# Kernel optimization log

Hardware: AMD Instinct MI355X
Metric: run time of the kernel (lower is better)

Reference implementation:

```python
import jax, jax.numpy as jnp
import numpy as np

B, T, D = 2, 1024, 1024   # batch, seq, d_model
E, F = 8, 4096            # n_experts, expert hidden (4*d_model)


def setup_inputs() -> dict:
    key = jax.random.key(0)
    k1, k2, k3, k4, k5 = jax.random.split(key, 5)
    x = jax.random.normal(k1, (B, T, D), dtype=jnp.float32)
    token_mask = jax.random.randint(k2, (B, T), 0, 2).astype(jnp.int32)
    router_w = jax.random.normal(k3, (E, D), dtype=jnp.float32) * (1.0 / np.sqrt(D))
    w1 = jax.random.normal(k4, (E, D, F), dtype=jnp.float32) * (1.0 / np.sqrt(D))
    w2 = jax.random.normal(k5, (E, F, D), dtype=jnp.float32) * (1.0 / np.sqrt(F))
    return {"x": x, "token_mask": token_mask, "router_w": router_w, "w1": w1, "w2": w2}


def reference(x, token_mask, router_w, w1, w2):
    b, t, d = x.shape
    n_exp = router_w.shape[0]
    xf = x.reshape(b * t, d)                       # [N, D]
    # top-1 router
    logits = xf @ router_w.T                       # [N, E]
    probs = jax.nn.softmax(logits, axis=-1)
    expert_idx = jnp.argmax(probs, axis=-1)        # [N]
    gate = jnp.take_along_axis(probs, expert_idx[:, None], axis=1)[:, 0]  # [N]
    # expert FFNs: each token routed to exactly one expert (dense masked combine)
    y = jnp.zeros_like(xf)
    for e in range(n_exp):
        he = jnp.maximum(xf @ w1[e], 0.0) @ w2[e]  # [N, D]
        y = jnp.where(expert_idx[:, None] == e, he, y)
    # gate scaling + token masking (masked rows stay exactly zero,
    # matching torch's zero-init y_flat_all + index_copy_)
    mask = token_mask.reshape(b * t).astype(x.dtype)
    out = y * (gate * mask)[:, None]
    return out.reshape(b, t, d)
```

## Files before the change

kernel.cpp:

```cpp
#include <hip/hip_runtime.h>
#include <hip/hip_bf16.h>

#define NTOK 2048
#define DM 1024
#define NEXP 8
#define FFN 4096
#define BM 64
#define BN 64
#define BK 64
#define ASTR 72
#define MT1 8
#define G2_SPLIT 4

typedef __bf16 bf16x8 __attribute__((ext_vector_type(8)));
typedef __bf16 bf16x4 __attribute__((ext_vector_type(4)));
typedef float f32x4 __attribute__((ext_vector_type(4)));

__device__ __forceinline__ bf16x8 zero8() {
  bf16x8 z;
#pragma unroll
  for (int j = 0; j < 8; j++) z[j] = (__bf16)0.f;
  return z;
}

__device__ __forceinline__ bf16x8 readB(const char* BsB, int row, int kh, int quad) {
  return *(const bf16x8*)(BsB + row * 144 +
                          ((((kh << 2) + quad) ^ (row >> 3)) << 4));
}

#define STOREB4() do {                                                   \
    const float* p0 = (const float*)&br0;                                \
    const float* p1 = (const float*)&br1;                                \
    const float* p2 = (const float*)&br2;                                \
    const float* p3 = (const float*)&br3;                                \
    _Pragma("unroll") for (int c = 0; c < 4; ++c) {                      \
      bf16x4 o;                                                          \
      o[0] = (__bf16)p0[c]; o[1] = (__bf16)p1[c];                        \
      o[2] = (__bf16)p2[c]; o[3] = (__bf16)p3[c];                        \
      *(bf16x4*)(bb + c * 144) = o;                                      \
    } } while (0)

__global__ __launch_bounds__(256) void router_gather(
    const float* __restrict__ x, const int* __restrict__ mask,
    const float* __restrict__ rw, int* __restrict__ counts,
    int* __restrict__ tlist, float* __restrict__ gateE,
    float* __restrict__ g_dense, __bf16* __restrict__ xg)
{
  int wid = threadIdx.x >> 6, lane = threadIdx.x & 63;
  int t = blockIdx.x * 4 + wid;

  const float* xr = x + (size_t)t * DM;
  float xv[16];
#pragma unroll
  for (int i = 0; i < 4; i++) {
    const float4 v = *(const float4*)(xr + lane * 16 + i * 4);
    xv[i * 4 + 0] = v.x; xv[i * 4 + 1] = v.y;
    xv[i * 4 + 2] = v.z; xv[i * 4 + 3] = v.w;
  }

  float acc[NEXP];
#pragma unroll
  for (int e = 0; e < NEXP; e++) {
    float a = 0.f;
    const float* rwe = rw + e * DM + lane * 16;
#pragma unroll
    for (int i = 0; i < 4; i++) {
      const float4 r = *(const float4*)(rwe + i * 4);
      a += xv[i*4+0]*r.x + xv[i*4+1]*r.y + xv[i*4+2]*r.z + xv[i*4+3]*r.w;
    }
    acc[e] = a;
  }
#pragma unroll
  for (int e = 0; e < NEXP; e++)
#pragma unroll
    for (int s = 1; s < 64; s <<= 1) acc[e] += __shfl_xor(acc[e], s, 64);

  int pack = -1;
  if (lane == 0 && mask[t] != 0) {
    float m = acc[0]; int am = 0;
#pragma unroll
    for (int e = 1; e < NEXP; e++) if (acc[e] > m) { m = acc[e]; am = e; }
    float s = 0.f;
#pragma unroll
    for (int e = 0; e < NEXP; e++) s += __expf(acc[e] - m);
    int slot = atomicAdd(&counts[am], 1);
    tlist[am * NTOK + slot] = t;
    float g = 1.0f / s;
    gateE[am * NTOK + slot] = g;
    g_dense[t] = g;
    pack = am * NTOK + slot;
  }
  pack = __shfl(pack, 0, 64);
  if (pack >= 0) {
    __bf16* dst = xg + (size_t)pack * DM + lane * 16;
    bf16x8 o0, o1;
#pragma unroll
    for (int j = 0; j < 8; j++) {
      o0[j] = (__bf16)xv[j];
      o1[j] = (__bf16)xv[8 + j];
    }
    *(bf16x8*)dst = o0;
    *(bf16x8*)(dst + 8) = o1;
  }
}

__global__ __launch_bounds__(256) void moe_gemm1(
    const __bf16* __restrict__ xg, const float* __restrict__ w1,
    const int* __restrict__ counts, const int* __restrict__ tlist,
    __bf16* __restrict__ h)
{
  int bx = blockIdx.x;
  int nt = bx & 63, mt = (bx >> 6) & (MT1 - 1), e = bx >> 9;
  int cnt = counts[e];
  if (mt * BM >= cnt) return;
  int n0 = nt * BN;

  __shared__ __bf16 As[BM][ASTR];
  __shared__ char   Bs[64 * 144];
  __shared__ int    toks[BM];

  int tid = threadIdx.x, lane = tid & 63, w = tid >> 6;
  int wm = w >> 1, wn = w & 1;
  int r16 = lane & 15, quad = lane >> 4;
  int rsw = r16 >> 1;
  char* bb = Bs + (r16 << 2) * 144 +
             (((((w << 1) + (quad >> 1))) ^ rsw) << 4) + ((quad & 1) << 3);

  const __bf16* xge = xg + (size_t)e * NTOK * DM;
  const float*  w1e = w1 + (size_t)e * DM * FFN;

  int ar = tid >> 2;
  int ak = (tid & 3) << 4;
  const float* bptr = w1e + (size_t)(w * 16 + quad * 4) * FFN + n0 + (r16 << 2);

  bf16x8 a0r, a1r;
  float4 br0, br1, br2, br3;

#define LOADG1(kb) do {                                                   \
    a0r = av ? *(const bf16x8*)(aptr + (kb))     : zero8();               \
    a1r = av ? *(const bf16x8*)(aptr + (kb) + 8) : zero8();               \
    br0 = *(const float4*)(bptr + (size_t)((kb) + 0) * FFN);              \
    br1 = *(const float4*)(bptr + (size_t)((kb) + 1) * FFN);              \
    br2 = *(const float4*)(bptr + (size_t)((kb) + 2) * FFN);              \
    br3 = *(const float4*)(bptr + (size_t)((kb) + 3) * FFN);              \
  } while (0)

  for (int m0 = mt * BM; m0 < cnt; m0 += MT1 * BM) {
    bool av = (m0 + ar) < cnt;
    const __bf16* aptr = xge + (size_t)(m0 + ar) * DM + ak;

    f32x4 acc[2][2] = {};
    LOADG1(0);
    const int T = DM / BK;
    for (int t = 0; t < T; t++) {
      *(bf16x8*)&As[ar][ak]     = a0r;
      *(bf16x8*)&As[ar][ak + 8] = a1r;
      STOREB4();
      __syncthreads();
      if (t + 1 < T) LOADG1((t + 1) * BK);
#pragma unroll
      for (int kh = 0; kh < 2; kh++) {
        int ks = kh * 32 + (quad << 3);
        bf16x8 aA = *(const bf16x8*)&As[wm * 32 + r16][ks];
        bf16x8 aB = *(const bf16x8*)&As[wm * 32 + 16 + r16][ks];
        bf16x8 bA = readB(Bs, wn * 32 + r16, kh, quad);
        bf16x8 bB = readB(Bs, wn * 32 + 16 + r16, kh, quad);
        acc[0][0] = __builtin_amdgcn_mfma_f32_16x16x32_bf16(aA, bA, acc[0][0], 0, 0, 0);
        acc[0][1] = __builtin_amdgcn_mfma_f32_16x16x32_bf16(aA, bB, acc[0][1], 0, 0, 0);
        acc[1][0] = __builtin_amdgcn_mfma_f32_16x16x32_bf16(aB, bA, acc[1][0], 0, 0, 0);
        acc[1][1] = __builtin_amdgcn_mfma_f32_16x16x32_bf16(aB, bB, acc[1][1], 0, 0, 0);
      }
      __syncthreads();
    }

    if (tid < BM) toks[tid] = (m0 + tid < cnt) ? tlist[e * NTOK + m0 + tid] : -1;
    __syncthreads();

#pragma unroll
    for (int mf = 0; mf < 2; mf++) {
#pragma unroll
      for (int i = 0; i < 4; i++) {
        int row = wm * 32 + mf * 16 + (quad << 2) + i;
        int tok = toks[row];
        if (tok >= 0) {
          __bf16* hp = h + (size_t)tok * FFN + n0 + wn * 32 + r16;
          hp[0]  = (__bf16)fmaxf(acc[mf][0][i], 0.f);
          hp[16] = (__bf16)fmaxf(acc[mf][1][i], 0.f);
        }
      }
    }
    __syncthreads();
  }
#undef LOADG1
}

__global__ __launch_bounds__(256) void moe_gemm2(
    const __bf16* __restrict__ h, const float* __restrict__ w2,
    const int* __restrict__ counts, const int* __restrict__ tlist,
    float* __restrict__ part)
{
  int bx = blockIdx.x;
  int nt = bx & 15, mt = (bx >> 4) & (MT1 - 1), e = (bx >> 7) & 7, sp = bx >> 10;
  int cnt = counts[e];
  if (mt * BM >= cnt) return;
  int n0 = nt * BN;
  int ksp = sp * (FFN / G2_SPLIT);

  __shared__ __bf16 As[BM][ASTR];
  __shared__ char   Bs[64 * 144];
  __shared__ int    toks[BM];

  int tid = threadIdx.x, lane = tid & 63, w = tid >> 6;
  int wm = w >> 1, wn = w & 1;
  int r16 = lane & 15, quad = lane >> 4;
  int rsw = r16 >> 1;
  char* bb = Bs + (r16 << 2) * 144 +
             (((((w << 1) + (quad >> 1))) ^ rsw) << 4) + ((quad & 1) << 3);

  const float* w2e = w2 + (size_t)e * FFN * DM;
  int ar = tid >> 2;
  int ak = (tid & 3) << 4;
  const float* bptr = w2e + (size_t)(ksp + w * 16 + quad * 4) * DM + n0 + (r16 << 2);
  float* psp = part + (size_t)sp * NTOK * DM;

  bf16x8 a0r, a1r;
  float4 br0, br1, br2, br3;

#define LOADG2(kb) do {                                                   \
    a0r = av ? *(const bf16x8*)(aptr + (kb))     : zero8();               \
    a1r = av ? *(const bf16x8*)(aptr + (kb) + 8) : zero8();               \
    br0 = *(const float4*)(bptr + (size_t)((kb) + 0) * DM);               \
    br1 = *(const float4*)(bptr + (size_t)((kb) + 1) * DM);               \
    br2 = *(const float4*)(bptr + (size_t)((kb) + 2) * DM);               \
    br3 = *(const float4*)(bptr + (size_t)((kb) + 3) * DM);               \
  } while (0)

  for (int m0 = mt * BM; m0 < cnt; m0 += MT1 * BM) {
    if (tid < BM) {
      toks[tid] = (m0 + tid < cnt) ? tlist[e * NTOK + m0 + tid] : -1;
    }
    __syncthreads();

    int tok0 = toks[ar];
    bool av = tok0 >= 0;
    const __bf16* aptr = h + (size_t)(av ? tok0 : 0) * FFN + ksp + ak;

    f32x4 acc[2][2] = {};
    LOADG2(0);
    const int T = (FFN / G2_SPLIT) / BK;
    for (int t = 0; t < T; t++) {
      *(bf16x8*)&As[ar][ak]     = a0r;
      *(bf16x8*)&As[ar][ak + 8] = a1r;
      STOREB4();
      __syncthreads();
      if (t + 1 < T) LOADG2((t + 1) * BK);
#pragma unroll
      for (int kh = 0; kh < 2; kh++) {
        int ks = kh * 32 + (quad << 3);
        bf16x8 aA = *(const bf16x8*)&As[wm * 32 + r16][ks];
        bf16x8 aB = *(const bf16x8*)&As[wm * 32 + 16 + r16][ks];
        bf16x8 bA = readB(Bs, wn * 32 + r16, kh, quad);
        bf16x8 bB = readB(Bs, wn * 32 + 16 + r16, kh, quad);
        acc[0][0] = __builtin_amdgcn_mfma_f32_16x16x32_bf16(aA, bA, acc[0][0], 0, 0, 0);
        acc[0][1] = __builtin_amdgcn_mfma_f32_16x16x32_bf16(aA, bB, acc[0][1], 0, 0, 0);
        acc[1][0] = __builtin_amdgcn_mfma_f32_16x16x32_bf16(aB, bA, acc[1][0], 0, 0, 0);
        acc[1][1] = __builtin_amdgcn_mfma_f32_16x16x32_bf16(aB, bB, acc[1][1], 0, 0, 0);
      }
      __syncthreads();
    }

#pragma unroll
    for (int mf = 0; mf < 2; mf++) {
#pragma unroll
      for (int i = 0; i < 4; i++) {
        int row = wm * 32 + mf * 16 + (quad << 2) + i;
        int tok = toks[row];
        if (tok >= 0) {
          float* pp = psp + (size_t)tok * DM + n0 + wn * 32 + r16;
          pp[0]  = acc[mf][0][i];
          pp[16] = acc[mf][1][i];
        }
      }
    }
    __syncthreads();
  }
#undef LOADG2
}

__global__ __launch_bounds__(256) void reduce4(
    const float* __restrict__ part, const float* __restrict__ gd,
    float* __restrict__ out)
{
  int i = blockIdx.x * 256 + threadIdx.x;
  const size_t SPSTRIDE = (size_t)NTOK * DM / 4;
  const float4* p = (const float4*)part;
  float4 a = p[i];
  float4 b = p[i + SPSTRIDE];
  float4 c = p[i + 2 * SPSTRIDE];
  float4 d = p[i + 3 * SPSTRIDE];
  float g = gd[i >> 8];
  float4 r;
  r.x = g * (a.x + b.x + c.x + d.x);
  r.y = g * (a.y + b.y + c.y + d.y);
  r.z = g * (a.z + b.z + c.z + d.z);
  r.w = g * (a.w + b.w + c.w + d.w);
  ((float4*)out)[i] = r;
}

extern "C" void kernel_launch(void* const* d_in, const int* in_sizes, int n_in,
                              void* d_out, int out_size, void* d_ws, size_t ws_size,
                              hipStream_t stream) {
  const float* x    = (const float*)d_in[0];
  const int*   mask = (const int*)d_in[1];
  const float* rw   = (const float*)d_in[2];
  const float* w1   = (const float*)d_in[3];
  const float* w2   = (const float*)d_in[4];
  float* out = (float*)d_out;

  char* ws = (char*)d_ws;
  int*    counts  = (int*)ws;
  int*    tlist   = (int*)(ws + 1024);
  float*  gateE   = (float*)(ws + 1024 + 65536);
  float*  g_dense = (float*)(ws + 1024 + 131072);
  __bf16* xg      = (__bf16*)(ws + 140544);
  __bf16* h       = (__bf16*)(ws + 140544 +
                              (size_t)NEXP * NTOK * DM * 2);
  float*  part    = (float*)(ws + 140544 +
                             (size_t)NEXP * NTOK * DM * 2 +
                             (size_t)NTOK * FFN * 2);

  hipMemsetAsync(counts, 0, 1024, stream);
  hipMemsetAsync(g_dense, 0, NTOK * sizeof(float), stream);

  router_gather<<<NTOK / 4, 256, 0, stream>>>(x, mask, rw, counts, tlist, gateE,
                                              g_dense, xg);
  moe_gemm1<<<NEXP * MT1 * (FFN / BN), 256, 0, stream>>>(xg, w1, counts, tlist, h);
  moe_gemm2<<<G2_SPLIT * NEXP * MT1 * (DM / BN), 256, 0, stream>>>(
      h, w2, counts, tlist, part);
  reduce4<<<NTOK * DM / 4 / 256, 256, 0, stream>>>(part, g_dense, out);
}
```

Before: 134.1 us.

## Store hidden activations expert-compacted and rebalance GEMM2 split-K grid

Hidden activations from the first GEMM are now written contiguously per expert, at an offset from a new prefix-scan kernel, instead of scattered by token index. The second GEMM then reads A rows contiguously without an indirect token lookup. GEMM2 moves from split-K 4 with 8 M-tiles to split-K 8 with 4 M-tiles, which changes how work is spread across CUs. The reduction now sums 8 partials, doubling the partial-buffer traffic, and an extra tiny kernel launch is added.

```diff
diff --git a/kernel.cpp b/kernel.cpp
--- a/kernel.cpp
+++ b/kernel.cpp
@@ -10,7 +10,8 @@
 #define BK 64
 #define ASTR 72
 #define MT1 8
-#define G2_SPLIT 4
+#define MT2 4
+#define G2_SPLIT 8
 
 typedef __bf16 bf16x8 __attribute__((ext_vector_type(8)));
 typedef __bf16 bf16x4 __attribute__((ext_vector_type(4)));
@@ -43,8 +44,8 @@
 __global__ __launch_bounds__(256) void router_gather(
     const float* __restrict__ x, const int* __restrict__ mask,
     const float* __restrict__ rw, int* __restrict__ counts,
-    int* __restrict__ tlist, float* __restrict__ gateE,
-    float* __restrict__ g_dense, __bf16* __restrict__ xg)
+    int* __restrict__ tlist, float* __restrict__ g_dense,
+    __bf16* __restrict__ xg)
 {
   int wid = threadIdx.x >> 6, lane = threadIdx.x & 63;
   int t = blockIdx.x * 4 + wid;
@@ -85,9 +86,7 @@
     for (int e = 0; e < NEXP; e++) s += __expf(acc[e] - m);
     int slot = atomicAdd(&counts[am], 1);
     tlist[am * NTOK + slot] = t;
-    float g = 1.0f / s;
-    gateE[am * NTOK + slot] = g;
-    g_dense[t] = g;
+    g_dense[t] = 1.0f / s;
     pack = am * NTOK + slot;
   }
   pack = __shfl(pack, 0, 64);
@@ -104,20 +103,28 @@
   }
 }
 
+__global__ void scan_offs(const int* __restrict__ counts, int* __restrict__ offs) {
+  if (threadIdx.x == 0) {
+    int s = 0;
+#pragma unroll
+    for (int e = 0; e < NEXP; e++) { offs[e] = s; s += counts[e]; }
+  }
+}
+
 __global__ __launch_bounds__(256) void moe_gemm1(
     const __bf16* __restrict__ xg, const float* __restrict__ w1,
-    const int* __restrict__ counts, const int* __restrict__ tlist,
-    __bf16* __restrict__ h)
+    const int* __restrict__ counts, const int* __restrict__ offs,
+    __bf16* __restrict__ hc)
 {
   int bx = blockIdx.x;
   int nt = bx & 63, mt = (bx >> 6) & (MT1 - 1), e = bx >> 9;
   int cnt = counts[e];
   if (mt * BM >= cnt) return;
   int n0 = nt * BN;
+  int hbase = offs[e];
 
   __shared__ __bf16 As[BM][ASTR];
   __shared__ char   Bs[64 * 144];
-  __shared__ int    toks[BM];
 
   int tid = threadIdx.x, lane = tid & 63, w = tid >> 6;
   int wm = w >> 1, wn = w & 1;
@@ -173,38 +180,34 @@
       __syncthreads();
     }
 
-    if (tid < BM) toks[tid] = (m0 + tid < cnt) ? tlist[e * NTOK + m0 + tid] : -1;
-    __syncthreads();
-
 #pragma unroll
     for (int mf = 0; mf < 2; mf++) {
 #pragma unroll
       for (int i = 0; i < 4; i++) {
         int row = wm * 32 + mf * 16 + (quad << 2) + i;
-        int tok = toks[row];
-        if (tok >= 0) {
-          __bf16* hp = h + (size_t)tok * FFN + n0 + wn * 32 + r16;
+        if (m0 + row < cnt) {
+          __bf16* hp = hc + (size_t)(hbase + m0 + row) * FFN + n0 + wn * 32 + r16;
           hp[0]  = (__bf16)fmaxf(acc[mf][0][i], 0.f);
           hp[16] = (__bf16)fmaxf(acc[mf][1][i], 0.f);
         }
       }
     }
-    __syncthreads();
   }
 #undef LOADG1
 }
 
 __global__ __launch_bounds__(256) void moe_gemm2(
-    const __bf16* __restrict__ h, const float* __restrict__ w2,
-    const int* __restrict__ counts, const int* __restrict__ tlist,
-    float* __restrict__ part)
+    const __bf16* __restrict__ hc, const float* __restrict__ w2,
+    const int* __restrict__ counts, const int* __restrict__ offs,
+    const int* __restrict__ tlist, float* __restrict__ part)
 {
   int bx = blockIdx.x;
-  int nt = bx & 15, mt = (bx >> 4) & (MT1 - 1), e = (bx >> 7) & 7, sp = bx >> 10;
+  int nt = bx & 15, mt = (bx >> 4) & (MT2 - 1), e = (bx >> 6) & 7, sp = bx >> 9;
   int cnt = counts[e];
   if (mt * BM >= cnt) return;
   int n0 = nt * BN;
   int ksp = sp * (FFN / G2_SPLIT);
+  int hbase = offs[e];
 
   __shared__ __bf16 As[BM][ASTR];
   __shared__ char   Bs[64 * 144];
@@ -235,15 +238,9 @@
     br3 = *(const float4*)(bptr + (size_t)((kb) + 3) * DM);               \
   } while (0)
 
-  for (int m0 = mt * BM; m0 < cnt; m0 += MT1 * BM) {
-    if (tid < BM) {
-      toks[tid] = (m0 + tid < cnt) ? tlist[e * NTOK + m0 + tid] : -1;
-    }
-    __syncthreads();
-
-    int tok0 = toks[ar];
-    bool av = tok0 >= 0;
-    const __bf16* aptr = h + (size_t)(av ? tok0 : 0) * FFN + ksp + ak;
+  for (int m0 = mt * BM; m0 < cnt; m0 += MT2 * BM) {
+    bool av = (m0 + ar) < cnt;
+    const __bf16* aptr = hc + (size_t)(hbase + (av ? m0 + ar : 0)) * FFN + ksp + ak;
 
     f32x4 acc[2][2] = {};
     LOADG2(0);
@@ -269,6 +266,9 @@
       __syncthreads();
     }
 
+    if (tid < BM) toks[tid] = (m0 + tid < cnt) ? tlist[e * NTOK + m0 + tid] : -1;
+    __syncthreads();
+
 #pragma unroll
     for (int mf = 0; mf < 2; mf++) {
 #pragma unroll
@@ -287,23 +287,22 @@
 #undef LOADG2
 }
 
-__global__ __launch_bounds__(256) void reduce4(
+__global__ __launch_bounds__(256) void reduce8(
     const float* __restrict__ part, const float* __restrict__ gd,
     float* __restrict__ out)
 {
   int i = blockIdx.x * 256 + threadIdx.x;
-  const size_t SPSTRIDE = (size_t)NTOK * DM / 4;
+  const size_t SPS = (size_t)NTOK * DM / 4;
   const float4* p = (const float4*)part;
-  float4 a = p[i];
-  float4 b = p[i + SPSTRIDE];
-  float4 c = p[i + 2 * SPSTRIDE];
-  float4 d = p[i + 3 * SPSTRIDE];
   float g = gd[i >> 8];
+  float sx = 0.f, sy = 0.f, sz = 0.f, sw = 0.f;
+#pragma unroll
+  for (int s = 0; s < G2_SPLIT; s++) {
+    float4 v = p[i + s * SPS];
+    sx += v.x; sy += v.y; sz += v.z; sw += v.w;
+  }
   float4 r;
-  r.x = g * (a.x + b.x + c.x + d.x);
-  r.y = g * (a.y + b.y + c.y + d.y);
-  r.z = g * (a.z + b.z + c.z + d.z);
-  r.w = g * (a.w + b.w + c.w + d.w);
+  r.x = g * sx; r.y = g * sy; r.z = g * sz; r.w = g * sw;
   ((float4*)out)[i] = r;
 }
 
@@ -319,23 +318,24 @@
 
   char* ws = (char*)d_ws;
   int*    counts  = (int*)ws;
-  int*    tlist   = (int*)(ws + 1024);
-  float*  gateE   = (float*)(ws + 1024 + 65536);
-  float*  g_dense = (float*)(ws + 1024 + 131072);
-  __bf16* xg      = (__bf16*)(ws + 140544);
-  __bf16* h       = (__bf16*)(ws + 140544 +
+  int*    offs    = (int*)(ws + 1024);
+  float*  g_dense = (float*)(ws + 2048);
+  int*    tlist   = (int*)(ws + 10240);
+  __bf16* xg      = (__bf16*)(ws + 131072);
+  __bf16* hc      = (__bf16*)(ws + 131072 +
                               (size_t)NEXP * NTOK * DM * 2);
-  float*  part    = (float*)(ws + 140544 +
+  float*  part    = (float*)(ws + 131072 +
                              (size_t)NEXP * NTOK * DM * 2 +
                              (size_t)NTOK * FFN * 2);
 
   hipMemsetAsync(counts, 0, 1024, stream);
   hipMemsetAsync(g_dense, 0, NTOK * sizeof(float), stream);
 
-  router_gather<<<NTOK / 4, 256, 0, stream>>>(x, mask, rw, counts, tlist, gateE,
+  router_gather<<<NTOK / 4, 256, 0, stream>>>(x, mask, rw, counts, tlist,
                                               g_dense, xg);
-  moe_gemm1<<<NEXP * MT1 * (FFN / BN), 256, 0, stream>>>(xg, w1, counts, tlist, h);
-  moe_gemm2<<<G2_SPLIT * NEXP * MT1 * (DM / BN), 256, 0, stream>>>(
-      h, w2, counts, tlist, part);
-  reduce4<<<NTOK * DM / 4 / 256, 256, 0, stream>>>(part, g_dense, out);
-}
+  scan_offs<<<1, 64, 0, stream>>>(counts, offs);
+  moe_gemm1<<<NEXP * MT1 * (FFN / BN), 256, 0, stream>>>(xg, w1, counts, offs, hc);
+  moe_gemm2<<<G2_SPLIT * NEXP * MT2 * (DM / BN), 256, 0, stream>>>(
+      hc, w2, counts, offs, tlist, part);
+  reduce8<<<NTOK * DM / 4 / 256, 256, 0, stream>>>(part, g_dense, out);
+}
```

Result: slower. 143.7 us (+7.2%).
